# Kernel optimization log

Hardware: AMD Instinct MI355X
Metric: run time of the kernel (lower is better)

## Reference

```python
import jax, jax.numpy as jnp
import numpy as np
import math

S, E, H, D, B, L = 16384, 1152, 16, 72, 16, 1024  # total tokens, embed, heads, head_dim, n_seqs, seq_len


def rotate_half(x):
    x1, x2 = jnp.split(x, 2, axis=-1)
    return jnp.concatenate((-x2, x1), axis=-1)


def setup_inputs() -> dict:
    key = jax.random.key(0)
    ks = jax.random.split(key, 8)
    hidden_states = jax.random.normal(ks[0], (S, E), jnp.float32)
    cu_seqlens = jnp.arange(B + 1, dtype=jnp.int32) * L  # equal-length segments (required by original reshape)
    ang = jax.random.uniform(ks[1], (S, D), jnp.float32, 0.0, 2.0 * math.pi)
    cos, sin = jnp.cos(ang), jnp.sin(ang)
    w = lambda k: jax.random.normal(k, (E, E), jnp.float32) * 0.02
    return {
        'hidden_states': hidden_states,
        'cu_seqlens': cu_seqlens,
        'cos': cos, 'sin': sin,
        'Wq': w(ks[2]), 'bq': jnp.zeros((E,), jnp.float32),
        'Wk': w(ks[3]), 'bk': jnp.zeros((E,), jnp.float32),
        'Wv': w(ks[4]), 'bv': jnp.zeros((E,), jnp.float32),
        'Wo': w(ks[5]), 'bo': jnp.zeros((E,), jnp.float32),
    }


def reference(hidden_states, cu_seqlens, cos, sin, Wq, bq, Wk, bk, Wv, bv, Wo, bo):
    seq_len, embed = hidden_states.shape
    q = (hidden_states @ Wq + bq).reshape(seq_len, H, D)
    k = (hidden_states @ Wk + bk).reshape(seq_len, H, D)
    v = (hidden_states @ Wv + bv).reshape(seq_len, H, D)
    # RoPE, broadcast over heads: cos/sin (S, 1, D)
    c = cos[:, None, :]
    s = sin[:, None, :]
    q = q * c + rotate_half(q) * s
    k = k * c + rotate_half(k) * s
    # varlen -> batched (equal-length segments; padding/mask is a no-op in this regime)
    nb = cu_seqlens.shape[0] - 1
    ls = seq_len // nb
    qb = q.reshape(nb, ls, H, D).transpose(0, 2, 1, 3)  # (B, H, L, D)
    kb = k.reshape(nb, ls, H, D).transpose(0, 2, 1, 3)
    vb = v.reshape(nb, ls, H, D).transpose(0, 2, 1, 3)
    scale = D ** -0.5
    scores = jnp.einsum('bhqd,bhkd->bhqk', qb, kb) * scale
    attn = jax.nn.softmax(scores, axis=-1)
    out = jnp.einsum('bhqk,bhkd->bhqd', attn, vb)
    out = out.transpose(0, 2, 1, 3).reshape(seq_len, embed)
    return out @ Wo + bo
```

## Files before the change

kernel.cpp:

```cpp
#include <hip/hip_runtime.h>

typedef __attribute__((ext_vector_type(8))) short bf16x8;
typedef __attribute__((ext_vector_type(4))) float f32x4;

#define S_LEN 16384
#define EMB   1152
#define NQKV  3456
#define NH    16
#define HD    72

__device__ __forceinline__ unsigned short f2b(float f){
  union { float f; unsigned u; } x; x.f = f;
  unsigned r = x.u + 0x7fffu + ((x.u >> 16) & 1u);
  return (unsigned short)(r >> 16);
}
__device__ __forceinline__ float b2f(unsigned short h){
  union { unsigned u; float f; } x; x.u = ((unsigned)h) << 16; return x.f;
}
__device__ __forceinline__ void glds16(const void* g, void* l){
  __builtin_amdgcn_global_load_lds((const __attribute__((address_space(1))) void*)g,
                                   (__attribute__((address_space(3))) void*)l, 16, 0, 0);
}

__global__ void prep_hs(const float* __restrict__ hs, unsigned short* __restrict__ hsb){
  long i = (long)blockIdx.x*256 + threadIdx.x;
  const long n8 = (long)S_LEN*EMB/8;
  if (i >= n8) return;
  const float4* p = (const float4*)(hs + i*8);
  float4 a = p[0], b = p[1];
  uint4 o;
  o.x = f2b(a.x) | ((unsigned)f2b(a.y)<<16);
  o.y = f2b(a.z) | ((unsigned)f2b(a.w)<<16);
  o.z = f2b(b.x) | ((unsigned)f2b(b.y)<<16);
  o.w = f2b(b.z) | ((unsigned)f2b(b.w)<<16);
  *(uint4*)(hsb + i*8) = o;
}

__global__ void prep_w(const float* __restrict__ Wq, const float* __restrict__ Wk,
                       const float* __restrict__ Wv, const float* __restrict__ Wo,
                       const float* __restrict__ bq, const float* __restrict__ bk,
                       const float* __restrict__ bv,
                       unsigned short* __restrict__ wqkv, unsigned short* __restrict__ wot,
                       float* __restrict__ biasq){
  long i = (long)blockIdx.x*256 + threadIdx.x;
  if (i < NQKV)
    biasq[i] = (i < 1152) ? bq[i] : (i < 2304 ? bk[i-1152] : bv[i-2304]);
  if (i >= (long)4608*1152) return;
  int k  = (int)(i % 1152);
  int n  = (int)(i / 1152);
  int sel = n / 1152, nn = n % 1152;
  const float* W = (sel==0)?Wq:(sel==1)?Wk:(sel==2)?Wv:Wo;
  unsigned short v = f2b(W[(long)k*1152 + nn]);
  if (sel < 3) wqkv[(long)n*1152 + k] = v;
  else         wot [(long)nn*1152 + k] = v;
}

template<int OUTF32>
__global__ __launch_bounds__(256) void gemm_bt(
    const unsigned short* __restrict__ A,
    const unsigned short* __restrict__ Bt,
    const float* __restrict__ bias,
    unsigned short* __restrict__ Cb,
    float* __restrict__ Cf,
    int N, int K)
{
  __shared__ unsigned short As[128*64];
  __shared__ unsigned short Bs[128*64];
  int tid = threadIdx.x;
  int lane = tid & 63, wave = tid >> 6;
  int wm = wave >> 1, wn = wave & 1;
  long ar0 = (long)blockIdx.y * 128;
  long bc0 = (long)blockIdx.x * 128;
  const unsigned short* ag = A  + (ar0 + tid/8)*(long)K + (tid&7)*8;
  const unsigned short* bg = Bt + (bc0 + tid/8)*(long)K + (tid&7)*8;
  unsigned short* al = As + tid*8;
  unsigned short* bl = Bs + tid*8;
  f32x4 acc[4][4];
  #pragma unroll
  for (int mi=0;mi<4;mi++)
    #pragma unroll
    for (int ni=0;ni<4;ni++) acc[mi][ni] = (f32x4){0.f,0.f,0.f,0.f};
  int lr = lane & 15, lk = (lane>>4)*8;
  for (int k0=0; k0<K; k0+=64){
    __syncthreads();
    #pragma unroll
    for (int i=0;i<4;i++){
      glds16(ag + (long)i*32*K + k0, al + i*32*64);
      glds16(bg + (long)i*32*K + k0, bl + i*32*64);
    }
    __syncthreads();
    #pragma unroll
    for (int ks=0;ks<2;ks++){
      bf16x8 af[4], bfr[4];
      #pragma unroll
      for (int mi=0;mi<4;mi++) af[mi]  = *(const bf16x8*)&As[(wm*64+mi*16+lr)*64 + ks*32 + lk];
      #pragma unroll
      for (int ni=0;ni<4;ni++) bfr[ni] = *(const bf16x8*)&Bs[(wn*64+ni*16+lr)*64 + ks*32 + lk];
      #pragma unroll
      for (int mi=0;mi<4;mi++)
        #pragma unroll
        for (int ni=0;ni<4;ni++)
          acc[mi][ni] = __builtin_amdgcn_mfma_f32_16x16x32_bf16(af[mi], bfr[ni], acc[mi][ni], 0,0,0);
    }
  }
  int orow = (lane>>4)*4, ocol = lane & 15;
  #pragma unroll
  for (int mi=0;mi<4;mi++){
    long r0 = ar0 + wm*64 + mi*16 + orow;
    #pragma unroll
    for (int ni=0;ni<4;ni++){
      long c = bc0 + wn*64 + ni*16 + ocol;
      float bb = bias[c];
      #pragma unroll
      for (int r=0;r<4;r++){
        float v = acc[mi][ni][r] + bb;
        if (OUTF32) Cf[(r0+r)*(long)N + c] = v;
        else        Cb[(r0+r)*(long)N + c] = f2b(v);
      }
    }
  }
}

__global__ void rope_k(unsigned short* __restrict__ qkv,
                       const float* __restrict__ cs, const float* __restrict__ sn){
  long i = (long)blockIdx.x*256 + threadIdx.x;
  const long tot = 2L*S_LEN*NH*36;
  if (i >= tot) return;
  int d = (int)(i % 36); long t2 = i/36;
  int h = (int)(t2 % NH); long t3 = t2/NH;
  int s = (int)(t3 % S_LEN); int qk = (int)(t3 / S_LEN);
  long base = (long)s*NQKV + (long)qk*1152 + h*HD;
  float x1 = b2f(qkv[base + d]), x2 = b2f(qkv[base + d + 36]);
  float c1 = cs[(long)s*HD + d], c2 = cs[(long)s*HD + d + 36];
  float s1 = sn[(long)s*HD + d], s2 = sn[(long)s*HD + d + 36];
  qkv[base + d]      = f2b(x1*c1 - x2*s1);
  qkv[base + d + 36] = f2b(x2*c2 + x1*s2);
}

__global__ void transpose_v(const unsigned short* __restrict__ qkv, unsigned short* __restrict__ vt){
  __shared__ unsigned short t[64*72];
  int tid = threadIdx.x;
  int kt = blockIdx.x, bh = blockIdx.y;
  int b = bh >> 4, h = bh & 15;
  const unsigned short* src = qkv + ((long)b*1024 + (long)kt*64)*NQKV + 2304 + h*HD;
  #pragma unroll
  for (int i=0;i<3;i++){
    int idx = i*256 + tid;
    if (idx < 576){
      int r = idx/9, c = (idx%9)*8;
      *(uint4*)&t[r*72 + c] = *(const uint4*)&src[(long)r*NQKV + c];
    }
  }
  __syncthreads();
  unsigned short* dst = vt + (long)bh*HD*1024 + (long)kt*64;
  #pragma unroll
  for (int i=0;i<3;i++){
    int idx = i*256 + tid;
    if (idx < 576){
      int d = idx>>3, k8 = (idx&7)*8;
      unsigned short v[8];
      #pragma unroll
      for (int j=0;j<8;j++) v[j] = t[(k8+j)*72 + d];
      uint4 o;
      o.x = v[0] | ((unsigned)v[1]<<16);
      o.y = v[2] | ((unsigned)v[3]<<16);
      o.z = v[4] | ((unsigned)v[5]<<16);
      o.w = v[6] | ((unsigned)v[7]<<16);
      *(uint4*)&dst[(long)d*1024 + k8] = o;
    }
  }
}

__global__ __launch_bounds__(512, 1) void attn3_k(
    const unsigned short* __restrict__ qkv,
    const unsigned short* __restrict__ vt,
    unsigned short* __restrict__ aout)
{
  __shared__ unsigned short Ks[64*72 + 32];
  __shared__ unsigned short Vts[80*72];
  __shared__ unsigned short Pt[8][16*72];
  int tid = threadIdx.x, lane = tid & 63, w = tid >> 6;
  int G = lane >> 4, l15 = lane & 15;
  int bid = blockIdx.x;
  int wg = (bid & 7)*256 + (bid >> 3);
  int bh = wg >> 3, qt = wg & 7;
  int b = bh >> 4, h = bh & 15;

  const unsigned short* kgbase = qkv + ((long)b*1024)*NQKV + 1152 + h*HD;
  const unsigned short* vgbase = vt + (long)bh*HD*1024;

  int key0 = tid/9,        kc0 = (tid%9)*8;
  bool ex  = (tid < 64);
  int ki1  = 512 + tid;
  int key1 = ki1/9,        kc1 = (ki1%9)*8;
  long koff0 = (long)key0*NQKV + kc0;  int kdst0 = key0*72 + kc0;
  long koff1 = (long)key1*NQKV + kc1;  int kdst1 = key1*72 + kc1;
  int vd0 = tid>>3,        vc0 = (tid&7)*8;
  int vi1 = 512 + tid;
  int vd1 = vi1>>3,        vc1 = (vi1&7)*8;
  long voff0 = (long)vd0*1024 + vc0;   int vdst0 = vd0*72 + vc0;
  long voff1 = (long)vd1*1024 + vc1;   int vdst1 = vd1*72 + vc1;

  uint4 pf0, pf1, pf2, pf3;
  #define STAGE_ISSUE(KT) do { \
    const unsigned short* kg_ = kgbase + (long)(KT)*64*NQKV; \
    const unsigned short* vg_ = vgbase + (KT)*64; \
    pf0 = *(const uint4*)(kg_ + koff0); \
    pf2 = *(const uint4*)(vg_ + voff0); \
    if (ex){ pf1 = *(const uint4*)(kg_ + koff1); pf3 = *(const uint4*)(vg_ + voff1); } \
  } while(0)
  #define STAGE_WRITE() do { \
    *(uint4*)&Ks[kdst0]  = pf0; \
    *(uint4*)&Vts[vdst0] = pf2; \
    if (ex){ *(uint4*)&Ks[kdst1] = pf1; *(uint4*)&Vts[vdst1] = pf3; } \
  } while(0)

  const uint4 z4 = make_uint4(0,0,0,0);
  if (tid < 4)  *(uint4*)&Ks[64*72 + tid*8] = z4;
  if (tid < 72) *(uint4*)&Vts[72*72 + tid*8] = z4;

  long sq0 = (long)b*1024 + qt*128 + w*16;
  const unsigned short* qrow = qkv + (sq0 + l15)*NQKV + h*HD;
  bf16x8 qf[3];
  #pragma unroll
  for (int ds=0; ds<3; ds++){
    int d0 = ds*32 + 8*G;
    if (d0 <= 64) qf[ds] = *(const bf16x8*)(qrow + d0);
    else          qf[ds] = (bf16x8){0,0,0,0,0,0,0,0};
  }

  f32x4 oacc[5];
  #pragma unroll
  for (int nd=0; nd<5; nd++) oacc[nd] = (f32x4){0.f,0.f,0.f,0.f};
  float m = -1e30f, lsum = 0.f;
  const float SL = 0.11785113f * 1.44269504f;

  STAGE_ISSUE(0);
  STAGE_WRITE();
  __syncthreads();

  unsigned short* pw = Pt[w];

  for (int kt=0; kt<16; kt++){
    if (kt < 15) STAGE_ISSUE(kt+1);

    f32x4 sacc[4];
    #pragma unroll
    for (int ni=0; ni<4; ni++) sacc[ni] = (f32x4){0.f,0.f,0.f,0.f};
    #pragma unroll
    for (int ds=0; ds<3; ds++){
      #pragma unroll
      for (int ni=0; ni<4; ni++){
        bf16x8 kf = *(const bf16x8*)&Ks[(ni*16 + l15)*72 + ds*32 + 8*G];
        sacc[ni] = __builtin_amdgcn_mfma_f32_16x16x32_bf16(kf, qf[ds], sacc[ni], 0,0,0);
      }
    }

    float tm = -1e30f;
    #pragma unroll
    for (int ni=0; ni<4; ni++)
      #pragma unroll
      for (int r=0; r<4; r++) tm = fmaxf(tm, sacc[ni][r]);
    tm = fmaxf(tm, __shfl_xor(tm, 16));
    tm = fmaxf(tm, __shfl_xor(tm, 32));
    float mn = fmaxf(m, tm);
    float corr = __builtin_amdgcn_exp2f((m - mn)*SL);
    m = mn; lsum *= corr;
    float msl = m * SL;
    float rs = 0.f;
    #pragma unroll
    for (int ni=0; ni<4; ni++)
      #pragma unroll
      for (int r=0; r<4; r++){
        float p = __builtin_amdgcn_exp2f(__builtin_fmaf(sacc[ni][r], SL, -msl));
        sacc[ni][r] = p; rs += p;
      }
    rs += __shfl_xor(rs, 16);
    rs += __shfl_xor(rs, 32);
    lsum += rs;

    #pragma unroll
    for (int ni=0; ni<4; ni++){
      unsigned u0 = (unsigned)f2b(sacc[ni][0]) | ((unsigned)f2b(sacc[ni][1])<<16);
      unsigned u1 = (unsigned)f2b(sacc[ni][2]) | ((unsigned)f2b(sacc[ni][3])<<16);
      *(unsigned*)&pw[l15*72 + ni*16 + 4*G]     = u0;
      *(unsigned*)&pw[l15*72 + ni*16 + 4*G + 2] = u1;
    }

    float c0 = __shfl(corr, 4*G + 0);
    float c1 = __shfl(corr, 4*G + 1);
    float c2 = __shfl(corr, 4*G + 2);
    float c3 = __shfl(corr, 4*G + 3);
    #pragma unroll
    for (int nd=0; nd<5; nd++){
      oacc[nd][0] *= c0; oacc[nd][1] *= c1; oacc[nd][2] *= c2; oacc[nd][3] *= c3;
    }

    #pragma unroll
    for (int ks=0; ks<2; ks++){
      bf16x8 pA = *(const bf16x8*)&pw[l15*72 + ks*32 + 8*G];
      #pragma unroll
      for (int nd=0; nd<5; nd++){
        bf16x8 vf = *(const bf16x8*)&Vts[(nd*16 + l15)*72 + ks*32 + 8*G];
        oacc[nd] = __builtin_amdgcn_mfma_f32_16x16x32_bf16(pA, vf, oacc[nd], 0,0,0);
      }
    }

    if (kt < 15){
      __syncthreads();
      STAGE_WRITE();
      __syncthreads();
    }
  }

  float inv = 1.f / lsum;
  float i0 = __shfl(inv, 4*G + 0);
  float i1 = __shfl(inv, 4*G + 1);
  float i2 = __shfl(inv, 4*G + 2);
  float i3 = __shfl(inv, 4*G + 3);
  #pragma unroll
  for (int nd=0; nd<5; nd++){
    int d = nd*16 + l15;
    if (d < HD){
      long base = (sq0 + 4*G)*EMB + h*HD + d;
      aout[base        ] = f2b(oacc[nd][0]*i0);
      aout[base +   EMB] = f2b(oacc[nd][1]*i1);
      aout[base + 2*EMB] = f2b(oacc[nd][2]*i2);
      aout[base + 3*EMB] = f2b(oacc[nd][3]*i3);
    }
  }
  #undef STAGE_ISSUE
  #undef STAGE_WRITE
}

extern "C" void kernel_launch(void* const* d_in, const int* in_sizes, int n_in,
                              void* d_out, int out_size, void* d_ws, size_t ws_size,
                              hipStream_t stream){
  const float* hs = (const float*)d_in[0];
  const float* cs = (const float*)d_in[2];
  const float* sn = (const float*)d_in[3];
  const float* Wq = (const float*)d_in[4];
  const float* bq = (const float*)d_in[5];
  const float* Wk = (const float*)d_in[6];
  const float* bk = (const float*)d_in[7];
  const float* Wv = (const float*)d_in[8];
  const float* bv = (const float*)d_in[9];
  const float* Wo = (const float*)d_in[10];
  const float* bo = (const float*)d_in[11];
  float* out = (float*)d_out;

  char* ws = (char*)d_ws;
  size_t off = 0;
  unsigned short* hsb  = (unsigned short*)(ws + off); off += (size_t)S_LEN*EMB*2;
  unsigned short* wqkv = (unsigned short*)(ws + off); off += (size_t)NQKV*EMB*2;
  unsigned short* wot  = (unsigned short*)(ws + off); off += (size_t)EMB*EMB*2;
  float*          biasq= (float*)(ws + off);          off += (size_t)NQKV*4 + 2560;
  unsigned short* qkv  = (unsigned short*)(ws + off); off += (size_t)S_LEN*NQKV*2;
  unsigned short* vt   = (unsigned short*)(ws + off); off += (size_t)256*HD*1024*2;

  prep_hs<<<(S_LEN*EMB/8 + 255)/256, 256, 0, stream>>>(hs, hsb);
  prep_w<<<((long)4608*1152 + 255)/256, 256, 0, stream>>>(Wq, Wk, Wv, Wo, bq, bk, bv, wqkv, wot, biasq);
  gemm_bt<0><<<dim3(NQKV/128, S_LEN/128), 256, 0, stream>>>(hsb, wqkv, biasq, qkv, nullptr, NQKV, EMB);
  rope_k<<<(2L*S_LEN*NH*36 + 255)/256, 256, 0, stream>>>(qkv, cs, sn);
  transpose_v<<<dim3(16, 256), 256, 0, stream>>>(qkv, vt);
  attn3_k<<<2048, 512, 0, stream>>>(qkv, vt, hsb);
  gemm_bt<1><<<dim3(EMB/128, S_LEN/128), 256, 0, stream>>>(hsb, wot, bo, nullptr, out, EMB, EMB);
}
```

Baseline: 695.9 us.

## Rewrite projection GEMMs with triple-buffered LDS pipeline, 256x128 tiles, swizzles

Replaces the 128x128 single-buffered GEMM with a 512-thread, 256x128-tile kernel. It prefetches two K-steps ahead into three LDS buffers using async global-to-LDS loads and vmcnt waits, so there is one barrier per K-step instead of two. It XOR-swizzles the LDS layout to avoid bank conflicts and remaps block IDs on a 1D grid for cache locality. The intent is to hide global-load latency in both the QKV and output projections. In exchange it uses more LDS per block (about 144 KB), which limits occupancy.

```diff
diff --git a/kernel.cpp b/kernel.cpp
--- a/kernel.cpp
+++ b/kernel.cpp
@@ -56,54 +56,96 @@
 }
 
 template<int OUTF32>
-__global__ __launch_bounds__(256) void gemm_bt(
+__global__ __launch_bounds__(512, 2) void gemm8(
     const unsigned short* __restrict__ A,
     const unsigned short* __restrict__ Bt,
     const float* __restrict__ bias,
     unsigned short* __restrict__ Cb,
     float* __restrict__ Cf,
-    int N, int K)
+    int N, int K, int NXT)
 {
-  __shared__ unsigned short As[128*64];
-  __shared__ unsigned short Bs[128*64];
-  int tid = threadIdx.x;
-  int lane = tid & 63, wave = tid >> 6;
+  __shared__ unsigned short lds[3*24576];
+  const int BUFE = 24576;
+  int tid = threadIdx.x, lane = tid & 63, wave = tid >> 6;
   int wm = wave >> 1, wn = wave & 1;
-  long ar0 = (long)blockIdx.y * 128;
-  long bc0 = (long)blockIdx.x * 128;
-  const unsigned short* ag = A  + (ar0 + tid/8)*(long)K + (tid&7)*8;
-  const unsigned short* bg = Bt + (bc0 + tid/8)*(long)K + (tid&7)*8;
-  unsigned short* al = As + tid*8;
-  unsigned short* bl = Bs + tid*8;
+  int lr = lane & 15, hi = lane >> 4, rx = lr & 7;
+
+  int nblk = gridDim.x, bid = blockIdx.x;
+  int cpx = nblk >> 3;
+  int swz = (bid & 7)*cpx + (bid >> 3);
+  long ar0 = (long)(swz / NXT) * 256;
+  long bc0 = (long)(swz % NXT) * 128;
+
+  const unsigned short* srcp[6];
+  int dsto[6];
+  #pragma unroll
+  for (int i=0;i<6;i++){
+    int f = i*512 + tid;
+    dsto[i] = f*8;
+    if (i < 4){
+      int row = f >> 3, cL = f & 7;
+      srcp[i] = A + (ar0 + row)*(long)K + (cL ^ (row & 7))*8;
+    } else {
+      int fb = f - 2048;
+      int row = fb >> 3, cL = fb & 7;
+      srcp[i] = Bt + (bc0 + row)*(long)K + (cL ^ (row & 7))*8;
+    }
+  }
+
+  int aoff[4][2], boff[4][2];
+  #pragma unroll
+  for (int mi=0;mi<4;mi++)
+    #pragma unroll
+    for (int ks=0;ks<2;ks++)
+      aoff[mi][ks] = (wm*64 + mi*16 + lr)*64 + (((ks*4 + hi) ^ rx)*8);
+  #pragma unroll
+  for (int ni=0;ni<4;ni++)
+    #pragma unroll
+    for (int ks=0;ks<2;ks++)
+      boff[ni][ks] = 16384 + (wn*64 + ni*16 + lr)*64 + (((ks*4 + hi) ^ rx)*8);
+
   f32x4 acc[4][4];
   #pragma unroll
   for (int mi=0;mi<4;mi++)
     #pragma unroll
     for (int ni=0;ni<4;ni++) acc[mi][ni] = (f32x4){0.f,0.f,0.f,0.f};
-  int lr = lane & 15, lk = (lane>>4)*8;
-  for (int k0=0; k0<K; k0+=64){
-    __syncthreads();
-    #pragma unroll
-    for (int i=0;i<4;i++){
-      glds16(ag + (long)i*32*K + k0, al + i*32*64);
-      glds16(bg + (long)i*32*K + k0, bl + i*32*64);
-    }
-    __syncthreads();
+
+  const int nT = K >> 6;
+  auto STG = [&](int T){
+    unsigned short* lb_ = lds + (T % 3)*BUFE;
+    long k0_ = (long)T * 64;
+    #pragma unroll
+    for (int i=0;i<6;i++) glds16(srcp[i] + k0_, lb_ + dsto[i]);
+  };
+
+  STG(0); STG(1);
+  asm volatile("s_waitcnt vmcnt(6)" ::: "memory");
+  __builtin_amdgcn_s_barrier();
+
+  for (int t=0; t<nT; ++t){
+    if (t+2 < nT) STG(t+2);
+    const unsigned short* lb = lds + (t % 3)*BUFE;
     #pragma unroll
     for (int ks=0;ks<2;ks++){
-      bf16x8 af[4], bfr[4];
-      #pragma unroll
-      for (int mi=0;mi<4;mi++) af[mi]  = *(const bf16x8*)&As[(wm*64+mi*16+lr)*64 + ks*32 + lk];
-      #pragma unroll
-      for (int ni=0;ni<4;ni++) bfr[ni] = *(const bf16x8*)&Bs[(wn*64+ni*16+lr)*64 + ks*32 + lk];
+      bf16x8 af[4], bfv[4];
+      #pragma unroll
+      for (int mi=0;mi<4;mi++) af[mi]  = *(const bf16x8*)(lb + aoff[mi][ks]);
+      #pragma unroll
+      for (int ni=0;ni<4;ni++) bfv[ni] = *(const bf16x8*)(lb + boff[ni][ks]);
       #pragma unroll
       for (int mi=0;mi<4;mi++)
         #pragma unroll
         for (int ni=0;ni<4;ni++)
-          acc[mi][ni] = __builtin_amdgcn_mfma_f32_16x16x32_bf16(af[mi], bfr[ni], acc[mi][ni], 0,0,0);
-    }
-  }
-  int orow = (lane>>4)*4, ocol = lane & 15;
+          acc[mi][ni] = __builtin_amdgcn_mfma_f32_16x16x32_bf16(af[mi], bfv[ni], acc[mi][ni], 0,0,0);
+    }
+    if (t+1 < nT){
+      if (t+2 < nT) asm volatile("s_waitcnt vmcnt(6)" ::: "memory");
+      else          asm volatile("s_waitcnt vmcnt(0)" ::: "memory");
+      __builtin_amdgcn_s_barrier();
+    }
+  }
+
+  int orow = hi*4, ocol = lr;
   #pragma unroll
   for (int mi=0;mi<4;mi++){
     long r0 = ar0 + wm*64 + mi*16 + orow;
@@ -360,9 +402,9 @@
 
   prep_hs<<<(S_LEN*EMB/8 + 255)/256, 256, 0, stream>>>(hs, hsb);
   prep_w<<<((long)4608*1152 + 255)/256, 256, 0, stream>>>(Wq, Wk, Wv, Wo, bq, bk, bv, wqkv, wot, biasq);
-  gemm_bt<0><<<dim3(NQKV/128, S_LEN/128), 256, 0, stream>>>(hsb, wqkv, biasq, qkv, nullptr, NQKV, EMB);
+  gemm8<0><<<dim3((NQKV/128)*(S_LEN/256)), 512, 0, stream>>>(hsb, wqkv, biasq, qkv, nullptr, NQKV, EMB, NQKV/128);
   rope_k<<<(2L*S_LEN*NH*36 + 255)/256, 256, 0, stream>>>(qkv, cs, sn);
   transpose_v<<<dim3(16, 256), 256, 0, stream>>>(qkv, vt);
   attn3_k<<<2048, 512, 0, stream>>>(qkv, vt, hsb);
-  gemm_bt<1><<<dim3(EMB/128, S_LEN/128), 256, 0, stream>>>(hsb, wot, bo, nullptr, out, EMB, EMB);
-}
+  gemm8<1><<<dim3((EMB/128)*(S_LEN/256)), 512, 0, stream>>>(hsb, wot, bo, nullptr, out, EMB, EMB, EMB/128);
+}
```

Result: faster. 614.2 us (-11.7%).
